# Kernel tuning notes

Measured on AMD Instinct MI355X. Metric: run time of the kernel, lower is better.

The kernel has to match this reference:

```python
import jax, jax.numpy as jnp
from jax import lax
import numpy as np

DECAY = 0.5   # LIF membrane leak factor
VTH = 1.0     # firing threshold


def _conv(x, w, stride, pad):
    # x: [B,C,H,W], w: [O,I,kh,kw]
    return lax.conv_general_dilated(
        x, w, (stride, stride), [(pad, pad), (pad, pad)],
        dimension_numbers=('NCHW', 'OIHW', 'NCHW'))


def _convT(x, w, b, stride=2, pad=1):
    # torch ConvTranspose2d(in,out,k,stride,pad): w is [Cin,Cout,k,k]
    k = w.shape[-1]
    wf = jnp.flip(w, (-2, -1)).transpose(1, 0, 2, 3)  # -> [Cout,Cin,k,k]
    y = lax.conv_general_dilated(
        x, wf, (1, 1), [(k - 1 - pad, k - 1 - pad)] * 2,
        lhs_dilation=(stride, stride),
        dimension_numbers=('NCHW', 'OIHW', 'NCHW'))
    return y + b[None, :, None, None]


def setup_inputs() -> dict:
    key = jax.random.key(0)
    ks = jax.random.split(key, 8)
    T, B = 16, 32
    x_seq = (jax.random.uniform(ks[0], (T, B, 1, 100, 368)) < 0.1).astype(jnp.float32)

    def p(k, shape, fan_in):
        return jax.random.normal(k, shape, jnp.float32) * (1.0 / np.sqrt(fan_in))

    return {
        'x_seq': x_seq,
        'w1': p(ks[1], (16, 1, 5, 5), 25),
        'w2': p(ks[2], (32, 16, 3, 3), 16 * 9),
        'wd': p(ks[3], (64, 32, 3, 3), 32 * 9),
        'bd': jnp.zeros((64,), jnp.float32),
        'wt1': p(ks[4], (64, 32, 4, 4), 64 * 16),
        'bt1': jnp.zeros((32,), jnp.float32),
        'wt2': p(ks[5], (32, 2, 4, 4), 32 * 16),
        'bt2': jnp.zeros((2,), jnp.float32),
        'actual_batch_size': 32,
    }


def reference(x_seq, w1, w2, wd, bd, wt1, bt1, wt2, bt2, actual_batch_size):
    B = x_seq.shape[1]
    dt = x_seq.dtype
    mem1 = jnp.zeros((B, 16, 50, 184), dt)
    mem2 = jnp.zeros((B, 32, 25, 92), dt)

    def step(carry, x):
        m1, m2 = carry
        # spiking conv layer 1: leaky integrate, fire, hard reset
        m1 = m1 * DECAY + _conv(x, w1, 2, 2)
        s1 = (m1 >= VTH).astype(dt)
        m1 = m1 * (1.0 - s1)
        # spiking conv layer 2 (return_dense -> membrane kept for decoder)
        m2 = m2 * DECAY + _conv(s1, w2, 2, 1)
        s2 = (m2 >= VTH).astype(dt)
        m2 = m2 * (1.0 - s2)
        return (m1, m2), None

    (mem1, mem2), _ = lax.scan(step, (mem1, mem2), x_seq)

    # dense CNN decoder on final membrane state
    h = jax.nn.relu(_conv(mem2, wd, 1, 1) + bd[None, :, None, None])   # [B,64,25,92]
    h = jax.nn.relu(_convT(h, wt1, bt1))                               # [B,32,50,184]
    out = jax.nn.softplus(_convT(h, wt2, bt2))                         # [B,2,100,368]
    inv_tau_c_pred = out[:, 0:1]
    alpha_pred = out[:, 1:2]
    return inv_tau_c_pred, alpha_pred
```

## Files before the change

kernel.cpp:

```cpp
#include <hip/hip_runtime.h>
#include <hip/hip_bf16.h>
#include <cstddef>


#define T_STEPS 16
#define NB 32
#define H0 100
#define W0 368
#define C1 16
#define H1 50
#define W1 184
#define C2 32
#define H2 25
#define W2 92
#define CD 64
#define WPR 6
#define SITES2 2300
#define SITES1 9200
#define NPOS1 (NB * H1 * W1)

using f32x16 = __attribute__((ext_vector_type(16))) float;
using f32x4  = __attribute__((ext_vector_type(4))) float;
using s16x8  = __attribute__((ext_vector_type(8))) short;

__device__ inline unsigned short f2bf(float f) {
    union { float f; unsigned int u; } v; v.f = f;
    unsigned int r = v.u + 0x7fffu + ((v.u >> 16) & 1u);
    return (unsigned short)(r >> 16);
}
__device__ inline float bf2f(unsigned short u) {
    union { unsigned int u; float f; } v; v.u = ((unsigned int)u) << 16;
    return v.f;
}
__device__ inline unsigned int pk2(float a, float b) {
    return (unsigned int)f2bf(a) | ((unsigned int)f2bf(b) << 16);
}
__device__ inline s16x8 ld8(const void* p) { return *reinterpret_cast<const s16x8*>(p); }

__global__ __launch_bounds__(256) void k_pack(const float* __restrict__ x,
                                              unsigned long long* __restrict__ xb) {
    int widx = blockIdx.x * 4 + (threadIdx.x >> 6);
    int lane = threadIdx.x & 63;
    int rowid = widx / WPR;
    int wcol  = widx - rowid * WPR;
    int col = (wcol << 6) + lane;
    const float* rp = x + (size_t)rowid * W0;
    float v = 0.f;
    if (col < W0) v = rp[col];
    unsigned long long m = __ballot(v != 0.f);
    if (lane == 0) xb[widx] = m;
}

__global__ __launch_bounds__(256) void k_mask(const unsigned long long* __restrict__ xb,
                                              unsigned int* __restrict__ bm) {
    int gid = blockIdx.x * blockDim.x + threadIdx.x;
    int t = gid / NPOS1;
    int site = gid - t * NPOS1;
    int x1 = site % W1;
    int tq = site / W1;
    int y1 = tq % H1;
    int b  = tq / H1;
    const int iy0 = 2 * y1 - 2;
    const int ix0 = 2 * x1 - 2;
    const int wi = ix0 >> 6;
    const int sh = ix0 & 63;
    const unsigned long long* xp = xb + ((size_t)(t * NB + b) * H0) * WPR;
    unsigned int bits25 = 0;
#pragma unroll
    for (int ky = 0; ky < 5; ++ky) {
        int iy = iy0 + ky;
        if (iy < 0 || iy >= H0) continue;
        const unsigned long long* row = xp + (size_t)iy * WPR;
        unsigned long long a = (wi >= 0) ? row[wi] : 0ull;
        unsigned long long bw = (wi + 1 < WPR) ? row[wi + 1] : 0ull;
        unsigned long long chunk = a >> sh;
        if (sh) chunk |= (bw << (64 - sh));
        bits25 |= ((unsigned int)chunk & 31u) << (5 * ky);
    }
    bm[gid] = bits25;
}

__global__ __launch_bounds__(256) void k_snn1(const unsigned int* __restrict__ bm,
                                              const unsigned short* __restrict__ w1b3,
                                              unsigned char* __restrict__ s1b) {
    __shared__ uint4 lut[256];
    {
        int m = (int)threadIdx.x;
        unsigned int wv[4];
#pragma unroll
        for (int h = 0; h < 4; ++h) {
            unsigned int lo = (m >> (2 * h)) & 1u, hb = (m >> (2 * h + 1)) & 1u;
            wv[h] = (lo ? 0x3F80u : 0u) | (hb ? 0x3F800000u : 0u);
        }
        lut[m] = make_uint4(wv[0], wv[1], wv[2], wv[3]);
    }
    __syncthreads();

    int wave = threadIdx.x >> 6;
    int lane = threadIdx.x & 63;
    int col = lane & 15;
    int hi  = lane >> 4;
    int base = (blockIdx.x * 4 + wave) * 64;

    s16x8 af0 = ld8((const char*)w1b3 + (size_t)((0 * 16 + col) * 32 + hi * 8) * 2);
    s16x8 af1 = ld8((const char*)w1b3 + (size_t)((1 * 16 + col) * 32 + hi * 8) * 2);
    s16x8 af2 = ld8((const char*)w1b3 + (size_t)((2 * 16 + col) * 32 + hi * 8) * 2);

    f32x4 acc0 = {}, acc1 = {}, acc2 = {}, acc3 = {};

    unsigned int cm0, cm1, cm2, cm3;
    {
        const unsigned int* bp = bm + base;
        cm0 = bp[col]; cm1 = bp[16 + col]; cm2 = bp[32 + col]; cm3 = bp[48 + col];
    }

    for (int t = 0; t < T_STEPS; ++t) {
        unsigned int nm0 = 0, nm1 = 0, nm2 = 0, nm3 = 0;
        if (t < T_STEPS - 1) {
            const unsigned int* bp = bm + (size_t)(t + 1) * NPOS1 + base;
            nm0 = bp[col]; nm1 = bp[16 + col]; nm2 = bp[32 + col]; nm3 = bp[48 + col];
        }
#pragma unroll
        for (int e = 0; e < 4; ++e) {
            acc0[e] *= 0.5f; acc1[e] *= 0.5f; acc2[e] *= 0.5f; acc3[e] *= 0.5f;
        }
#pragma unroll
        for (int g = 0; g < 4; ++g) {
            unsigned int sb = (g == 0) ? cm0 : (g == 1) ? cm1 : (g == 2) ? cm2 : cm3;
            unsigned int byte = (sb >> (hi * 8)) & 0xFFu;
            s16x8 bf = *reinterpret_cast<const s16x8*>(&lut[byte]);
            f32x4& ac = (g == 0) ? acc0 : (g == 1) ? acc1 : (g == 2) ? acc2 : acc3;
            ac = __builtin_amdgcn_mfma_f32_16x16x32_bf16(af0, bf, ac, 0, 0, 0);
            ac = __builtin_amdgcn_mfma_f32_16x16x32_bf16(af1, bf, ac, 0, 0, 0);
            ac = __builtin_amdgcn_mfma_f32_16x16x32_bf16(af2, bf, ac, 0, 0, 0);
        }
#pragma unroll
        for (int g = 0; g < 4; ++g) {
            f32x4& ac = (g == 0) ? acc0 : (g == 1) ? acc1 : (g == 2) ? acc2 : acc3;
            unsigned int nib = 0;
#pragma unroll
            for (int e = 0; e < 4; ++e) {
                float v = ac[e];
                bool s = (v >= 1.0f);
                if (s) nib |= (1u << e);
                ac[e] = s ? 0.f : v;
            }
            unsigned int mk = nib << ((hi & 1) * 4);
            mk |= __shfl_xor(mk, 16, 64);
            if (hi == 0)
                s1b[(size_t)(t * 2 + 0) * NPOS1 + base + g * 16 + col] = (unsigned char)mk;
            else if (hi == 2)
                s1b[(size_t)(t * 2 + 1) * NPOS1 + base + g * 16 + col] = (unsigned char)mk;
        }
        cm0 = nm0; cm1 = nm1; cm2 = nm2; cm3 = nm3;
    }
}

__global__ __launch_bounds__(256, 1) void k_snn2(const unsigned char* __restrict__ s1b,
                                                 const unsigned short* __restrict__ w2b3,
                                                 unsigned short* __restrict__ mem2bf) {
    __shared__ uint4 lut[256];
    {
        int m = (int)threadIdx.x;
        unsigned int wv[4];
#pragma unroll
        for (int h = 0; h < 4; ++h) {
            unsigned int lo = (m >> (2 * h)) & 1u, hb = (m >> (2 * h + 1)) & 1u;
            wv[h] = (lo ? 0x3F80u : 0u) | (hb ? 0x3F800000u : 0u);
        }
        lut[m] = make_uint4(wv[0], wv[1], wv[2], wv[3]);
    }
    __syncthreads();

    int wave = threadIdx.x >> 6;
    int lane = threadIdx.x & 63;
    int col = lane & 31, hi = lane >> 5;
    int gsite = (blockIdx.x * 4 + wave) * 32 + col;
    int b = gsite / SITES2;
    int rest = gsite % SITES2;
    int y2 = rest / W2, x2 = rest % W2;

    int toff[9]; bool tval[9];
#pragma unroll
    for (int ky = 0; ky < 3; ++ky)
#pragma unroll
        for (int kx = 0; kx < 3; ++kx) {
            int iy = 2 * y2 + ky - 1, ix = 2 * x2 + kx - 1;
            tval[ky * 3 + kx] = iy >= 0 && iy < H1 && ix >= 0 && ix < W1;
            toff[ky * 3 + kx] = iy * W1 + ix;
        }

    const char* ab = (const char*)w2b3;
    s16x8 a0[9], a1[9], a2[9];
#pragma unroll
    for (int s = 0; s < 9; ++s) {
        int ko = (s * 16 + hi * 8) * 2;
        a0[s] = ld8(ab + (col * 144) * 2 + ko);
        a1[s] = ld8(ab + ((32 + col) * 144) * 2 + ko);
        a2[s] = ld8(ab + ((64 + col) * 144) * 2 + ko);
    }

    f32x16 acc = {};

    unsigned int msk[9];
    {
        const unsigned char* spk = s1b + (size_t)hi * NPOS1 + (size_t)b * (H1 * W1);
#pragma unroll
        for (int i = 0; i < 9; ++i)
            msk[i] = tval[i] ? (unsigned int)spk[toff[i]] : 0u;
    }

    for (int t = 0; t < T_STEPS; ++t) {
        unsigned int nmsk[9];
#pragma unroll
        for (int i = 0; i < 9; ++i) nmsk[i] = 0u;
        if (t < T_STEPS - 1) {
            const unsigned char* spk = s1b + (size_t)((t + 1) * 2 + hi) * NPOS1 + (size_t)b * (H1 * W1);
#pragma unroll
            for (int i = 0; i < 9; ++i)
                nmsk[i] = tval[i] ? (unsigned int)spk[toff[i]] : 0u;
        }

        s16x8 bfr[9];
#pragma unroll
        for (int s = 0; s < 9; ++s)
            bfr[s] = *reinterpret_cast<const s16x8*>(&lut[msk[s]]);

#pragma unroll
        for (int e = 0; e < 16; ++e) acc[e] *= 0.5f;

#pragma unroll
        for (int s = 0; s < 9; ++s) {
            acc = __builtin_amdgcn_mfma_f32_32x32x16_bf16(a0[s], bfr[s], acc, 0, 0, 0);
            acc = __builtin_amdgcn_mfma_f32_32x32x16_bf16(a1[s], bfr[s], acc, 0, 0, 0);
            acc = __builtin_amdgcn_mfma_f32_32x32x16_bf16(a2[s], bfr[s], acc, 0, 0, 0);
        }
#pragma unroll
        for (int e = 0; e < 16; ++e) {
            float v = acc[e];
            acc[e] = (v >= 1.0f) ? 0.f : v;
        }
#pragma unroll
        for (int i = 0; i < 9; ++i) msk[i] = nmsk[i];
    }

    char* obase = (char*)(mem2bf + (size_t)gsite * C2);
#pragma unroll
    for (int q = 0; q < 4; ++q) {
        int co = 8 * q + 4 * hi;
        uint2 u;
        u.x = pk2(acc[4 * q + 0], acc[4 * q + 1]);
        u.y = pk2(acc[4 * q + 2], acc[4 * q + 3]);
        *(uint2*)(obase + co * 2) = u;
    }
}

__global__ __launch_bounds__(256) void k_repackb(const float* __restrict__ wd,
                                                 const float* __restrict__ wt1,
                                                 const float* __restrict__ wt2,
                                                 const float* __restrict__ w2,
                                                 const float* __restrict__ w1,
                                                 unsigned short* __restrict__ wdb,
                                                 unsigned short* __restrict__ wt1b,
                                                 float* __restrict__ wt2k,
                                                 unsigned short* __restrict__ w2b3,
                                                 unsigned short* __restrict__ w1b3) {
    int gid = blockIdx.x * blockDim.x + threadIdx.x;
    if (gid < 64 * 288) {
        int co = gid / 288, k = gid % 288;
        int tap = k >> 5, ci = k & 31;
        wdb[gid] = f2bf(wd[((size_t)co * C2 + ci) * 9 + tap]);
    } else if (gid < 64 * 288 + 4 * 32 * 256) {
        int j = gid - 64 * 288;
        int par = j >> 13, co = (j >> 8) & 31, k = j & 255;
        int tap = k >> 6, ci = k & 63;
        int ty = tap >> 1, tx = tap & 1;
        int ry = par >> 1, rx = par & 1;
        int ky = ry ? (ty ? 0 : 2) : (ty ? 3 : 1);
        int kx = rx ? (tx ? 0 : 2) : (tx ? 3 : 1);
        wt1b[j] = f2bf(wt1[(((size_t)ci * 32 + co) * 4 + ky) * 4 + kx]);
    } else if (gid < 64 * 288 + 4 * 32 * 256 + 1024) {
        int j = gid - (64 * 288 + 4 * 32 * 256);
        int par = j >> 8, tap = (j >> 6) & 3, ci = (j >> 1) & 31, co = j & 1;
        int ty = tap >> 1, tx = tap & 1;
        int ry = par >> 1, rx = par & 1;
        int ky = ry ? (ty ? 0 : 2) : (ty ? 3 : 1);
        int kx = rx ? (tx ? 0 : 2) : (tx ? 3 : 1);
        wt2k[j] = wt2[(((size_t)ci * 2 + co) * 4 + ky) * 4 + kx];
    } else if (gid < 64 * 288 + 4 * 32 * 256 + 1024 + 3 * 32 * 144) {
        int j = gid - (64 * 288 + 4 * 32 * 256 + 1024);
        int p = j / 4608, rem = j % 4608;
        int co = rem / 144, k = rem % 144;
        int tap = k / 16, ci = k % 16;
        float w = w2[((size_t)co * C1 + ci) * 9 + tap];
        unsigned short b0 = f2bf(w);
        float r1 = w - bf2f(b0);
        unsigned short b1 = f2bf(r1);
        float r2 = r1 - bf2f(b1);
        unsigned short b2 = f2bf(r2);
        w2b3[j] = (p == 0) ? b0 : (p == 1) ? b1 : b2;
    } else if (gid < 64 * 288 + 4 * 32 * 256 + 1024 + 3 * 32 * 144 + 3 * 16 * 32) {
        int j = gid - (64 * 288 + 4 * 32 * 256 + 1024 + 3 * 32 * 144);
        int p = j / 512, rem = j % 512;
        int co = rem / 32, k = rem % 32;
        float w = (k < 25) ? w1[co * 25 + k] : 0.f;
        unsigned short b0 = f2bf(w);
        float r1 = w - bf2f(b0);
        unsigned short b1 = f2bf(r1);
        float r2 = r1 - bf2f(b1);
        unsigned short b2 = f2bf(r2);
        w1b3[j] = (p == 0) ? b0 : (p == 1) ? b1 : b2;
    }
}

__global__ __launch_bounds__(256) void k_convd(const unsigned short* __restrict__ mem2bf,
                                               const unsigned short* __restrict__ wdb,
                                               const float* __restrict__ bd,
                                               unsigned short* __restrict__ h1bf) {
    int wave = threadIdx.x >> 6;
    int lane = threadIdx.x & 63;
    int col = lane & 31, hi = lane >> 5;
    int cog = blockIdx.y;
    int b = blockIdx.z;
    int n0 = (blockIdx.x * 4 + wave) * 32;
    int site = n0 + col;
    bool sval = site < SITES2;
    int sc = sval ? site : 0;
    int yy = sc / W2, xx = sc % W2;

    const char* ibase = (const char*)(mem2bf + (size_t)b * SITES2 * C2);
    int toff[9];
    bool tval[9];
#pragma unroll
    for (int ky = 0; ky < 3; ++ky)
#pragma unroll
        for (int kx = 0; kx < 3; ++kx) {
            int iy = yy + ky - 1, ix = xx + kx - 1;
            bool v = sval && iy >= 0 && iy < H2 && ix >= 0 && ix < W2;
            tval[ky * 3 + kx] = v;
            toff[ky * 3 + kx] = (iy * W2 + ix) * (C2 * 2);
        }

    const s16x8 zero = {0, 0, 0, 0, 0, 0, 0, 0};
    s16x8 bfr[18];
#pragma unroll
    for (int s = 0; s < 18; ++s) {
        int tap = s >> 1;
        int boff = (s & 1) * 32 + hi * 16;
        bfr[s] = tval[tap] ? ld8(ibase + toff[tap] + boff) : zero;
    }
    const char* abase = (const char*)wdb + (size_t)(cog * 32 + col) * 576 + hi * 16;
    s16x8 ar[18];
#pragma unroll
    for (int s = 0; s < 18; ++s)
        ar[s] = ld8(abase + s * 32);

    f32x16 acc = {};
#pragma unroll
    for (int s = 0; s < 18; ++s)
        acc = __builtin_amdgcn_mfma_f32_32x32x16_bf16(ar[s], bfr[s], acc, 0, 0, 0);

    if (!sval) return;
    char* obase = (char*)(h1bf + ((size_t)b * SITES2 + site) * CD);
#pragma unroll
    for (int q = 0; q < 4; ++q) {
        int co = cog * 32 + 8 * q + 4 * hi;
        float v0 = fmaxf(acc[4 * q + 0] + bd[co + 0], 0.f);
        float v1 = fmaxf(acc[4 * q + 1] + bd[co + 1], 0.f);
        float v2 = fmaxf(acc[4 * q + 2] + bd[co + 2], 0.f);
        float v3 = fmaxf(acc[4 * q + 3] + bd[co + 3], 0.f);
        uint2 u; u.x = pk2(v0, v1); u.y = pk2(v2, v3);
        *(uint2*)(obase + co * 2) = u;
    }
}

__global__ __launch_bounds__(256) void k_convt1(const unsigned short* __restrict__ h1bf,
                                                const unsigned short* __restrict__ wt1b,
                                                const float* __restrict__ bt1,
                                                unsigned short* __restrict__ h2bf) {
    int par = threadIdx.x >> 6;
    int lane = threadIdx.x & 63;
    int col = lane & 31, hi = lane >> 5;
    int ry = par >> 1, rx = par & 1;
    int b = blockIdx.z;
    int bx = blockIdx.x;
    int tile = (bx & 7) * 9 + (bx >> 3);
    int n0 = tile * 32;

    const char* ibase = (const char*)(h1bf + (size_t)b * SITES2 * CD);
    int site = n0 + col;
    bool sv = site < SITES2;
    int sc = sv ? site : 0;
    int m = sc / W2, n = sc % W2;
    int iy1 = m + (ry ? 1 : -1);
    int ix1 = n + (rx ? 1 : -1);
    bool y1v = iy1 >= 0 && iy1 < H2;
    bool x1v = ix1 >= 0 && ix1 < W2;
    int toff[4]; bool tval[4];
#pragma unroll
    for (int t = 0; t < 4; ++t) {
        int ty = t >> 1, tx = t & 1;
        int iy = ty ? iy1 : m;
        int ix = tx ? ix1 : n;
        tval[t] = sv && (ty ? y1v : true) && (tx ? x1v : true);
        toff[t] = (iy * W2 + ix) * (CD * 2);
    }

    const s16x8 zero = {0, 0, 0, 0, 0, 0, 0, 0};
    s16x8 bfr[16];
#pragma unroll
    for (int s = 0; s < 16; ++s) {
        int tap = s >> 2;
        int boff = (s & 3) * 32 + hi * 16;
        bfr[s] = tval[tap] ? ld8(ibase + toff[tap] + boff) : zero;
    }
    const char* abase = (const char*)(wt1b + (size_t)par * 32 * 256) + (size_t)col * 512 + hi * 16;
    s16x8 ar[16];
#pragma unroll
    for (int s = 0; s < 16; ++s)
        ar[s] = ld8(abase + s * 32);

    f32x16 acc = {};
#pragma unroll
    for (int s = 0; s < 16; ++s)
        acc = __builtin_amdgcn_mfma_f32_32x32x16_bf16(ar[s], bfr[s], acc, 0, 0, 0);

    if (!sv) return;
    int oy = 2 * m + ry, ox = 2 * n + rx;
    char* obase = (char*)(h2bf + ((size_t)b * SITES1 + (size_t)oy * W1 + ox) * C2);
#pragma unroll
    for (int q = 0; q < 4; ++q) {
        int co = 8 * q + 4 * hi;
        float v0 = fmaxf(acc[4 * q + 0] + bt1[co + 0], 0.f);
        float v1 = fmaxf(acc[4 * q + 1] + bt1[co + 1], 0.f);
        float v2 = fmaxf(acc[4 * q + 2] + bt1[co + 2], 0.f);
        float v3 = fmaxf(acc[4 * q + 3] + bt1[co + 3], 0.f);
        uint2 u; u.x = pk2(v0, v1); u.y = pk2(v2, v3);
        *(uint2*)(obase + co * 2) = u;
    }
}

__global__ __launch_bounds__(256) void k_convt2(const unsigned short* __restrict__ h2bf,
                                                const float* __restrict__ wt2k,
                                                const float* __restrict__ bt2,
                                                float* __restrict__ out) {
    int i = blockIdx.x * blockDim.x + threadIdx.x;
    if (i >= SITES1) return;
    int par = blockIdx.y;
    int ry = par >> 1, rx = par & 1;
    int b = blockIdx.z;
    int m = i / W1, n = i % W1;
    int iy1 = m + (ry ? 1 : -1);
    int ix1 = n + (rx ? 1 : -1);
    bool y1v = iy1 >= 0 && iy1 < H1;
    bool x1v = ix1 >= 0 && ix1 < W1;

    float a0 = bt2[0], a1 = bt2[1];
    const unsigned short* ib = h2bf + (size_t)b * SITES1 * C2;
#pragma unroll
    for (int t = 0; t < 4; ++t) {
        int ty = t >> 1, tx = t & 1;
        if ((ty && !y1v) || (tx && !x1v)) continue;
        int iy = ty ? iy1 : m;
        int ix = tx ? ix1 : n;
        const unsigned short* p = ib + ((size_t)iy * W1 + ix) * C2;
        const float* w = wt2k + ((size_t)par * 4 + t) * 64;
#pragma unroll
        for (int g = 0; g < 4; ++g) {
            s16x8 v8 = ld8(p + g * 8);
#pragma unroll
            for (int e = 0; e < 8; ++e) {
                float v = bf2f((unsigned short)v8[e]);
                int ci = g * 8 + e;
                a0 += v * w[2 * ci];
                a1 += v * w[2 * ci + 1];
            }
        }
    }
    int oy = 2 * m + ry, ox = 2 * n + rx;
    size_t base_o = (size_t)b * (H0 * W0) + (size_t)oy * W0 + ox;
    out[base_o] = fmaxf(a0, 0.f) + log1pf(expf(-fabsf(a0)));
    out[(size_t)NB * H0 * W0 + base_o] = fmaxf(a1, 0.f) + log1pf(expf(-fabsf(a1)));
}

extern "C" void kernel_launch(void* const* d_in, const int* in_sizes, int n_in,
                              void* d_out, int out_size, void* d_ws, size_t ws_size,
                              hipStream_t stream) {
    const float* x   = (const float*)d_in[0];
    const float* w1  = (const float*)d_in[1];
    const float* w2  = (const float*)d_in[2];
    const float* wd  = (const float*)d_in[3];
    const float* bd  = (const float*)d_in[4];
    const float* wt1 = (const float*)d_in[5];
    const float* bt1 = (const float*)d_in[6];
    const float* wt2 = (const float*)d_in[7];
    const float* bt2 = (const float*)d_in[8];
    float* out = (float*)d_out;

    char* ws = (char*)d_ws;
    unsigned char* s1b     = (unsigned char*)(ws);
    unsigned short* mem2bf = (unsigned short*)(ws + 9420800);
    unsigned short* h1bf   = (unsigned short*)(ws + 14131200);
    unsigned short* h2bf   = (unsigned short*)(ws + 23552000);
    unsigned long long* xb = (unsigned long long*)(ws + 42393600);
    unsigned short* wdb    = (unsigned short*)(ws + 44851200);
    unsigned short* wt1b   = (unsigned short*)(ws + 44888064);
    float* wt2k            = (float*)(ws + 44953600);
    unsigned short* w2b3   = (unsigned short*)(ws + 44957696);
    unsigned short* w1b3   = (unsigned short*)(ws + 44985344);
    unsigned int* bm       = (unsigned int*)(ws + 44988416);

    {
        int n = 64 * 288 + 4 * 32 * 256 + 1024 + 3 * 32 * 144 + 3 * 16 * 32;
        k_repackb<<<(n + 255) / 256, 256, 0, stream>>>(wd, wt1, wt2, w2, w1,
                                                       wdb, wt1b, wt2k, w2b3, w1b3);
    }
    {
        k_pack<<<76800, 256, 0, stream>>>(x, xb);
    }
    {
        k_mask<<<18400, 256, 0, stream>>>(xb, bm);
    }
    {
        k_snn1<<<1150, 256, 0, stream>>>(bm, w1b3, s1b);
    }
    {
        k_snn2<<<575, 256, 0, stream>>>(s1b, w2b3, mem2bf);
    }
    {
        dim3 g(18, 2, NB);
        k_convd<<<g, 256, 0, stream>>>(mem2bf, wdb, bd, h1bf);
    }
    {
        dim3 g(72, 1, NB);
        k_convt1<<<g, 256, 0, stream>>>(h1bf, wt1b, bt1, h2bf);
    }
    {
        dim3 g(36, 4, NB);
        k_convt2<<<g, 256, 0, stream>>>(h2bf, wt2k, bt2, out);
    }
}
```

Before: 208.4 us.

## Stage conv2 weights in LDS and split MFMA chain into three accumulators

Moves the 27 per-lane bf16 weight fragments of the layer-2 spiking conv from registers into a shared-memory table loaded once per block. The freed registers allow launch bounds of two blocks per CU. The single serial MFMA accumulation chain is split into three independent accumulators that are summed before thresholding, which removes the back-to-back dependency between MFMAs. In exchange, every MFMA now needs an LDS read of its A operand each timestep, and the extra accumulators use more VGPRs again.

```diff
diff --git a/kernel.cpp b/kernel.cpp
--- a/kernel.cpp
+++ b/kernel.cpp
@@ -156,10 +156,11 @@
     }
 }
 
-__global__ __launch_bounds__(256, 1) void k_snn2(const unsigned char* __restrict__ s1b,
+__global__ __launch_bounds__(256, 2) void k_snn2(const unsigned char* __restrict__ s1b,
                                                  const unsigned short* __restrict__ w2b3,
                                                  unsigned short* __restrict__ mem2bf) {
     __shared__ uint4 lut[256];
+    __shared__ uint4 wl[1728];
     {
         int m = (int)threadIdx.x;
         unsigned int wv[4];
@@ -169,6 +170,12 @@
             wv[h] = (lo ? 0x3F80u : 0u) | (hb ? 0x3F800000u : 0u);
         }
         lut[m] = make_uint4(wv[0], wv[1], wv[2], wv[3]);
+    }
+    for (int d = (int)threadIdx.x; d < 1728; d += 256) {
+        int f = d >> 6, l = d & 63;
+        int p = f / 9, s = f - p * 9;
+        const char* src = (const char*)w2b3 + p * 9216 + (l & 31) * 288 + s * 32 + (l >> 5) * 16;
+        wl[d] = *(const uint4*)src;
     }
     __syncthreads();
 
@@ -190,17 +197,9 @@
             toff[ky * 3 + kx] = iy * W1 + ix;
         }
 
-    const char* ab = (const char*)w2b3;
-    s16x8 a0[9], a1[9], a2[9];
-#pragma unroll
-    for (int s = 0; s < 9; ++s) {
-        int ko = (s * 16 + hi * 8) * 2;
-        a0[s] = ld8(ab + (col * 144) * 2 + ko);
-        a1[s] = ld8(ab + ((32 + col) * 144) * 2 + ko);
-        a2[s] = ld8(ab + ((64 + col) * 144) * 2 + ko);
-    }
-
-    f32x16 acc = {};
+    const s16x8* wlp = reinterpret_cast<const s16x8*>(wl);
+
+    f32x16 m = {};
 
     unsigned int msk[9];
     {
@@ -226,19 +225,19 @@
         for (int s = 0; s < 9; ++s)
             bfr[s] = *reinterpret_cast<const s16x8*>(&lut[msk[s]]);
 
-#pragma unroll
-        for (int e = 0; e < 16; ++e) acc[e] *= 0.5f;
-
+        f32x16 c0, c1 = {}, c2 = {};
+#pragma unroll
+        for (int e = 0; e < 16; ++e) c0[e] = m[e] * 0.5f;
 #pragma unroll
         for (int s = 0; s < 9; ++s) {
-            acc = __builtin_amdgcn_mfma_f32_32x32x16_bf16(a0[s], bfr[s], acc, 0, 0, 0);
-            acc = __builtin_amdgcn_mfma_f32_32x32x16_bf16(a1[s], bfr[s], acc, 0, 0, 0);
-            acc = __builtin_amdgcn_mfma_f32_32x32x16_bf16(a2[s], bfr[s], acc, 0, 0, 0);
+            c0 = __builtin_amdgcn_mfma_f32_32x32x16_bf16(wlp[(0 * 9 + s) * 64 + lane], bfr[s], c0, 0, 0, 0);
+            c1 = __builtin_amdgcn_mfma_f32_32x32x16_bf16(wlp[(1 * 9 + s) * 64 + lane], bfr[s], c1, 0, 0, 0);
+            c2 = __builtin_amdgcn_mfma_f32_32x32x16_bf16(wlp[(2 * 9 + s) * 64 + lane], bfr[s], c2, 0, 0, 0);
         }
 #pragma unroll
         for (int e = 0; e < 16; ++e) {
-            float v = acc[e];
-            acc[e] = (v >= 1.0f) ? 0.f : v;
+            float v = c0[e] + c1[e] + c2[e];
+            m[e] = (v >= 1.0f) ? 0.f : v;
         }
 #pragma unroll
         for (int i = 0; i < 9; ++i) msk[i] = nmsk[i];
@@ -249,8 +248,8 @@
     for (int q = 0; q < 4; ++q) {
         int co = 8 * q + 4 * hi;
         uint2 u;
-        u.x = pk2(acc[4 * q + 0], acc[4 * q + 1]);
-        u.y = pk2(acc[4 * q + 2], acc[4 * q + 3]);
+        u.x = pk2(m[4 * q + 0], m[4 * q + 1]);
+        u.y = pk2(m[4 * q + 2], m[4 * q + 3]);
         *(uint2*)(obase + co * 2) = u;
     }
 }
```

After: 219.0 us. +5.1%, slower.
